# Performance work log

Hardware: AMD Instinct MI355X
Metric: run time of the kernel (lower is better)

The kernel has to match this reference:

```python
import jax, jax.numpy as jnp
import numpy as np

DIM, HEADS, SEQ_LEN = 768, 12, 4096
HEAD_DIM = DIM // HEADS
RMS_EPS = 1.1920928955078125e-07  # torch fp32 finfo eps (default for F.rms_norm)
ATTN_SCALE = 0.12


def _rms_norm(x):
    # F.rms_norm(x, (x.size(-1),)) with no weight
    return x * jax.lax.rsqrt(jnp.mean(x * x, axis=-1, keepdims=True) + RMS_EPS)


def _rotary_tables(T, head_dim):
    # angular_freq: (1/1024)**linspace(0,1,head_dim//4) padded with zeros to head_dim//2
    freqs = (1.0 / 1024.0) ** jnp.linspace(0.0, 1.0, head_dim // 4, dtype=jnp.float32)
    freqs = jnp.concatenate([freqs, jnp.zeros(head_dim // 4, dtype=jnp.float32)])
    t = jnp.arange(T, dtype=jnp.float32)
    theta = t[:, None] * freqs[None, :]  # [T, head_dim//2]
    return jnp.cos(theta), jnp.sin(theta)


def _apply_rotary(x, cos, sin):
    # x: [B, T, H, D]; cos/sin: [T, D//2]
    x1, x2 = jnp.split(x.astype(jnp.float32), 2, axis=-1)
    c = cos[None, :, None, :]
    s = sin[None, :, None, :]
    y1 = x1 * c + x2 * s
    y2 = -x1 * s + x2 * c
    return jnp.concatenate([y1, y2], axis=-1).astype(x.dtype)


def setup_inputs() -> dict:
    key = jax.random.key(0)
    k1, k2, k3 = jax.random.split(key, 3)
    x = jax.random.normal(k1, (1, SEQ_LEN, DIM), dtype=jnp.float32)
    std = 0.5 * DIM ** (-0.5)
    bound = (3.0 ** 0.5) * std
    qkv_w = jax.random.uniform(k2, (3, DIM, DIM), dtype=jnp.float32, minval=-bound, maxval=bound)
    # c_proj is zero-initialized in the module; use small random weights for a nontrivial baseline
    c_proj_w = jax.random.normal(k3, (DIM, DIM), dtype=jnp.float32) * (DIM ** -0.5)
    return {"x": x, "qkv_w": qkv_w, "c_proj_w": c_proj_w}


def reference(x, qkv_w, c_proj_w):
    B, T, dim = x.shape
    H, D = HEADS, HEAD_DIM
    # fused QKV: F.linear(x, qkv_w.flatten(end_dim=1)) -> x @ W^T, split into q,k,v
    qkv = jnp.einsum('btd,kfd->btkf', x, qkv_w)  # [B, T, 3, dim]
    qkv = qkv.reshape(B, T, 3, H, D)
    q, k, v = qkv[:, :, 0], qkv[:, :, 1], qkv[:, :, 2]  # each [B, T, H, D]
    q, k = _rms_norm(q), _rms_norm(k)
    cos, sin = _rotary_tables(T, D)
    q, k = _apply_rotary(q, cos, sin), _apply_rotary(k, cos, sin)
    # causal attention with scale=0.12 (flex_attention with causal block mask)
    scores = jnp.einsum('bthd,bshd->bhts', q, k) * ATTN_SCALE  # [B, H, T, T]
    causal = jnp.tril(jnp.ones((T, T), dtype=bool))
    scores = jnp.where(causal[None, None], scores, jnp.finfo(scores.dtype).min)
    probs = jax.nn.softmax(scores, axis=-1)
    y = jnp.einsum('bhts,bshd->bthd', probs, v).reshape(B, T, dim)
    return y @ c_proj_w.T
```

## Files before the change

kernel.cpp:

```cpp
#include <hip/hip_runtime.h>
#include <math.h>


typedef __bf16 bf16;
typedef __bf16 bf16x4 __attribute__((ext_vector_type(4)));
typedef __bf16 bf16x8 __attribute__((ext_vector_type(8)));
typedef float  f32x4  __attribute__((ext_vector_type(4)));

#define MFMA_BF16(a, b, c) __builtin_amdgcn_mfma_f32_16x16x32_bf16((a), (b), (c), 0, 0, 0)

#define SEQ  4096
#define NH   12
#define HD   64
#define DM   768
#define NQKV 2304
#define NPART 4
#define ATTN_SCALE 0.12f
#define LOG2E 1.4426950408889634f
#define RMS_EPS 1.1920928955078125e-07f

typedef __attribute__((address_space(3))) void  lds_void;
typedef const __attribute__((address_space(1))) void g_void;

__device__ __forceinline__ void gload16(const void* g, void* l)
{
  __builtin_amdgcn_global_load_lds((g_void*)g, (lds_void*)l, 16, 0, 0);
}

__global__ __launch_bounds__(256) void convert_all(
    const float* __restrict__ s0, bf16* __restrict__ d0, int n0,
    const float* __restrict__ s1, bf16* __restrict__ d1, int n1,
    const float* __restrict__ s2, bf16* __restrict__ d2, int n2)
{
  int b = blockIdx.x;
  const int b0 = n0 >> 11, b1 = n1 >> 11;
  const float* s; bf16* d;
  if (b < b0)            { s = s0; d = d0; }
  else if (b < b0 + b1)  { s = s1; d = d1; b -= b0; }
  else                   { s = s2; d = d2; b -= b0 + b1; }
  const int i0 = (b * 256 + threadIdx.x) * 8;
  f32x4 a = *(const f32x4*)(s + i0);
  f32x4 c = *(const f32x4*)(s + i0 + 4);
  bf16x8 o;
#pragma unroll
  for (int j = 0; j < 4; j++) { o[j] = (bf16)a[j]; o[j + 4] = (bf16)c[j]; }
  *(bf16x8*)(d + i0) = o;
}

__device__ __forceinline__ void gemm128_core(
    const bf16* __restrict__ A, const bf16* __restrict__ B,
    int m0, int n0, bf16 (*As)[128][32], bf16 (*Bs)[128][32], f32x4 acc[4][4])
{
  const int tid = threadIdx.x;
  const int lane = tid & 63, w = tid >> 6;
  const int c16 = lane & 15, q4 = lane >> 4;
  const int mo = (w & 1) * 64, no = (w >> 1) * 64;
  const int srow = tid >> 2, scol = (tid & 3) * 8;
  const f32x4 vzero = {0.f, 0.f, 0.f, 0.f};
#pragma unroll
  for (int i = 0; i < 4; i++)
#pragma unroll
    for (int j = 0; j < 4; j++) acc[i][j] = vzero;

  const bf16* aBase = A + (size_t)(m0 + srow) * DM + scol;
  const bf16* bBase = B + (size_t)(n0 + srow) * DM + scol;

#define STAGE128(buf, kk) do {                                          \
    gload16(aBase + (kk),                   &As[buf][srow][scol]);      \
    gload16(aBase + (size_t)64 * DM + (kk), &As[buf][srow + 64][scol]); \
    gload16(bBase + (kk),                   &Bs[buf][srow][scol]);      \
    gload16(bBase + (size_t)64 * DM + (kk), &Bs[buf][srow + 64][scol]); \
  } while (0)

  STAGE128(0, 0);
  __syncthreads();
  int cur = 0;
  for (int k0 = 0; k0 < DM; k0 += 32) {
    const int kn = k0 + 32;
    if (kn < DM) STAGE128(cur ^ 1, kn);
    bf16x8 ar[4], br[4];
#pragma unroll
    for (int mq = 0; mq < 4; mq++)
      ar[mq] = *(const bf16x8*)&As[cur][mo + mq * 16 + c16][q4 * 8];
#pragma unroll
    for (int nq = 0; nq < 4; nq++)
      br[nq] = *(const bf16x8*)&Bs[cur][no + nq * 16 + c16][q4 * 8];
    __builtin_amdgcn_s_setprio(1);
#pragma unroll
    for (int mq = 0; mq < 4; mq++)
#pragma unroll
      for (int nq = 0; nq < 4; nq++)
        acc[mq][nq] = MFMA_BF16(ar[mq], br[nq], acc[mq][nq]);
    __builtin_amdgcn_s_setprio(0);
    __syncthreads();
    cur ^= 1;
  }
#undef STAGE128
}

__global__ __launch_bounds__(256) void gemm_qkv(
    const bf16* __restrict__ A, const bf16* __restrict__ B,
    bf16* __restrict__ Qb, bf16* __restrict__ Kb, bf16* __restrict__ Vt)
{
  __shared__ bf16 As[2][128][32];
  __shared__ bf16 Bs[2][128][32];
  const int m0 = blockIdx.x * 128, n0 = blockIdx.y * 128;
  f32x4 acc[4][4];
  gemm128_core(A, B, m0, n0, As, Bs, acc);

  const int lane = threadIdx.x & 63, w = threadIdx.x >> 6;
  const int c16 = lane & 15, q4 = lane >> 4;
  const int mo = (w & 1) * 64, no = (w >> 1) * 64;
  const int kidx = blockIdx.y / 6;
  const int rr0 = (n0 - kidx * DM) + no;
  const int h = rr0 >> 6;

  if (kidx == 2) {
#pragma unroll
    for (int nq = 0; nq < 4; nq++) {
      const int d = nq * 16 + c16;
#pragma unroll
      for (int mq = 0; mq < 4; mq++) {
        const int mb = m0 + mo + mq * 16 + q4 * 4;
#pragma unroll
        for (int rg = 0; rg < 4; rg++)
          Vt[((h * HD) + d) * SEQ + mb + rg] = (bf16)acc[mq][nq][rg];
      }
    }
  } else {
    bf16* dst = kidx ? Kb : Qb;
    const float scale = kidx ? 1.0f : (ATTN_SCALE * LOG2E);
    const float fr = exp2f(-10.0f * (float)c16 * (1.0f / 15.0f));
#pragma unroll
    for (int mq = 0; mq < 4; mq++) {
#pragma unroll
      for (int rg = 0; rg < 4; rg++) {
        const int m = m0 + mo + mq * 16 + q4 * 4 + rg;
        const float x0 = acc[mq][0][rg], x1 = acc[mq][1][rg];
        const float x2 = acc[mq][2][rg], x3 = acc[mq][3][rg];
        float ss = x0 * x0 + x1 * x1 + x2 * x2 + x3 * x3;
        ss += __shfl_xor(ss, 1, 64);
        ss += __shfl_xor(ss, 2, 64);
        ss += __shfl_xor(ss, 4, 64);
        ss += __shfl_xor(ss, 8, 64);
        const float rinv = rsqrtf(ss * (1.0f / 64.0f) + RMS_EPS) * scale;
        const float xn0 = x0 * rinv, xn1 = x1 * rinv;
        const float xn2 = x2 * rinv, xn3 = x3 * rinv;
        float sn, cs;
        sincosf((float)m * fr, &sn, &cs);
        const float y0 = xn0 * cs + xn2 * sn;
        const float y2 = xn2 * cs - xn0 * sn;
        bf16* rp = dst + (size_t)(h * SEQ + m) * HD + c16;
        rp[0]  = (bf16)y0;
        rp[16] = (bf16)xn1;
        rp[32] = (bf16)y2;
        rp[48] = (bf16)xn3;
      }
    }
  }
}

__global__ __launch_bounds__(256) void gemm_proj(
    const bf16* __restrict__ A, const bf16* __restrict__ B, float* __restrict__ C)
{
  __shared__ bf16 As[2][64][32];
  __shared__ bf16 Bs[2][64][32];
  const int m0 = blockIdx.x * 64, n0 = blockIdx.y * 64;
  const int tid = threadIdx.x;
  const int lane = tid & 63, w = tid >> 6;
  const int c16 = lane & 15, q4 = lane >> 4;
  const int mo = (w & 1) * 32, no = (w >> 1) * 32;
  const int srow = tid >> 2, scol = (tid & 3) * 8;
  const f32x4 vzero = {0.f, 0.f, 0.f, 0.f};
  f32x4 acc[2][2];
#pragma unroll
  for (int i = 0; i < 2; i++)
#pragma unroll
    for (int j = 0; j < 2; j++) acc[i][j] = vzero;

  const bf16* aBase = A + (size_t)(m0 + srow) * DM + scol;
  const bf16* bBase = B + (size_t)(n0 + srow) * DM + scol;

#define STAGE64(buf, kk) do {                          \
    gload16(aBase + (kk), &As[buf][srow][scol]);       \
    gload16(bBase + (kk), &Bs[buf][srow][scol]);       \
  } while (0)

  STAGE64(0, 0);
  __syncthreads();
  int cur = 0;
  for (int k0 = 0; k0 < DM; k0 += 32) {
    const int kn = k0 + 32;
    if (kn < DM) STAGE64(cur ^ 1, kn);
    bf16x8 ar[2], br[2];
#pragma unroll
    for (int mq = 0; mq < 2; mq++)
      ar[mq] = *(const bf16x8*)&As[cur][mo + mq * 16 + c16][q4 * 8];
#pragma unroll
    for (int nq = 0; nq < 2; nq++)
      br[nq] = *(const bf16x8*)&Bs[cur][no + nq * 16 + c16][q4 * 8];
    __builtin_amdgcn_s_setprio(1);
#pragma unroll
    for (int mq = 0; mq < 2; mq++)
#pragma unroll
      for (int nq = 0; nq < 2; nq++)
        acc[mq][nq] = MFMA_BF16(ar[mq], br[nq], acc[mq][nq]);
    __builtin_amdgcn_s_setprio(0);
    __syncthreads();
    cur ^= 1;
  }
#undef STAGE64

#pragma unroll
  for (int nq = 0; nq < 2; nq++) {
    const int n = n0 + no + nq * 16 + c16;
#pragma unroll
    for (int mq = 0; mq < 2; mq++) {
      const int mb = m0 + mo + mq * 16 + q4 * 4;
#pragma unroll
      for (int rg = 0; rg < 4; rg++)
        C[(size_t)(mb + rg) * DM + n] = acc[mq][nq][rg];
    }
  }
}

__global__ __launch_bounds__(256, 3) void flash_partial(
    const bf16* __restrict__ Qb, const bf16* __restrict__ Kb,
    const bf16* __restrict__ Vt, bf16* __restrict__ Opart,
    float* __restrict__ Lpart)
{
  __shared__ bf16 Ks[64][72];
  __shared__ bf16 Vts[64][72];
  __shared__ bf16 Pst[4][32][68];
  const int id = blockIdx.x;
  const int swz = (id & 7) * 96 + (id >> 3);
  const int h = swz >> 6;
  const int rrem = swz & 63;
  const int p = rrem >> 4;
  const int jb = rrem & 15;
  const int tid = threadIdx.x;
  const int lane = tid & 63, w = tid >> 6;
  const int c16 = lane & 15, q4 = lane >> 4;
  const int sr = tid >> 3, sc8 = (tid & 7) * 8;

  const bf16* Kbase = Kb + (size_t)h * SEQ * HD;
  const bf16* Vbase = Vt + (size_t)h * HD * SEQ;
  const f32x4 vzero = {0.f, 0.f, 0.f, 0.f};

#pragma unroll 1
  for (int half = 0; half < 2; ++half) {
    const int qi = half ? jb : (31 - jb);
    const int q0 = qi * 128;

    bf16x8 aq[2][2];
#pragma unroll
    for (int f = 0; f < 2; f++) {
      const int tq = q0 + w * 32 + f * 16 + c16;
      aq[f][0] = *(const bf16x8*)&Qb[((h * SEQ) + tq) * HD + q4 * 8];
      aq[f][1] = *(const bf16x8*)&Qb[((h * SEQ) + tq) * HD + 32 + q4 * 8];
    }
    const int qg[2] = { q0 + w * 32 + c16, q0 + w * 32 + 16 + c16 };
    const int qb[2] = { q0 + w * 32,       q0 + w * 32 + 16 };

    f32x4 O[2][4];
    float l_f[2] = {0.f, 0.f};
#pragma unroll
    for (int f = 0; f < 2; f++)
#pragma unroll
      for (int j = 0; j < 4; j++) O[f][j] = vzero;

    const int sEnd = q0 + 64;
    const int sBeg = p * 64;
    if (sBeg <= sEnd) {
      bf16x8 kr0 = *(const bf16x8*)&Kbase[(sBeg + sr) * HD + sc8];
      bf16x8 kr1 = *(const bf16x8*)&Kbase[(sBeg + sr + 32) * HD + sc8];
      bf16x8 vr0 = *(const bf16x8*)&Vbase[sr * SEQ + sBeg + sc8];
      bf16x8 vr1 = *(const bf16x8*)&Vbase[(sr + 32) * SEQ + sBeg + sc8];

      for (int s0 = sBeg; s0 <= sEnd; s0 += NPART * 64) {
        __syncthreads();
        *(bf16x8*)&Ks[sr][sc8]       = kr0;
        *(bf16x8*)&Ks[sr + 32][sc8]  = kr1;
        *(bf16x8*)&Vts[sr][sc8]      = vr0;
        *(bf16x8*)&Vts[sr + 32][sc8] = vr1;
        __syncthreads();

        const int snext = s0 + NPART * 64;
        if (snext <= sEnd) {
          kr0 = *(const bf16x8*)&Kbase[(snext + sr) * HD + sc8];
          kr1 = *(const bf16x8*)&Kbase[(snext + sr + 32) * HD + sc8];
          vr0 = *(const bf16x8*)&Vbase[sr * SEQ + snext + sc8];
          vr1 = *(const bf16x8*)&Vbase[(sr + 32) * SEQ + snext + sc8];
        }

        bf16x8 kf0[4], kf1[4];
#pragma unroll
        for (int nt = 0; nt < 4; nt++) {
          kf0[nt] = *(const bf16x8*)&Ks[nt * 16 + c16][q4 * 8];
          kf1[nt] = *(const bf16x8*)&Ks[nt * 16 + c16][32 + q4 * 8];
        }
#pragma unroll
        for (int f = 0; f < 2; f++) {
          f32x4 S[4];
          __builtin_amdgcn_s_setprio(1);
#pragma unroll
          for (int nt = 0; nt < 4; nt++) {
            f32x4 z = vzero;
            z = MFMA_BF16(kf0[nt], aq[f][0], z);
            z = MFMA_BF16(kf1[nt], aq[f][1], z);
            S[nt] = z;
          }
          __builtin_amdgcn_s_setprio(0);
          float lf = l_f[f];
          if (s0 + 63 <= qb[f]) {
#pragma unroll
            for (int nt = 0; nt < 4; nt++) {
#pragma unroll
              for (int rg = 0; rg < 4; rg++) {
                const float pv = exp2f(S[nt][rg]);
                S[nt][rg] = pv;
                lf += pv;
              }
              bf16x4 pk = { (bf16)S[nt][0], (bf16)S[nt][1], (bf16)S[nt][2], (bf16)S[nt][3] };
              *(bf16x4*)&Pst[w][f * 16 + c16][nt * 16 + q4 * 4] = pk;
            }
          } else if (s0 > qb[f] + 15) {
            const bf16x4 zk = { (bf16)0.f, (bf16)0.f, (bf16)0.f, (bf16)0.f };
#pragma unroll
            for (int nt = 0; nt < 4; nt++)
              *(bf16x4*)&Pst[w][f * 16 + c16][nt * 16 + q4 * 4] = zk;
          } else {
#pragma unroll
            for (int nt = 0; nt < 4; nt++) {
#pragma unroll
              for (int rg = 0; rg < 4; rg++) {
                const int s_g = s0 + nt * 16 + q4 * 4 + rg;
                const float pv = (s_g > qg[f]) ? 0.f : exp2f(S[nt][rg]);
                S[nt][rg] = pv;
                lf += pv;
              }
              bf16x4 pk = { (bf16)S[nt][0], (bf16)S[nt][1], (bf16)S[nt][2], (bf16)S[nt][3] };
              *(bf16x4*)&Pst[w][f * 16 + c16][nt * 16 + q4 * 4] = pk;
            }
          }
          l_f[f] = lf;
        }
        bf16x8 ap[2][2];
#pragma unroll
        for (int f = 0; f < 2; f++) {
          ap[f][0] = *(const bf16x8*)&Pst[w][f * 16 + c16][q4 * 8];
          ap[f][1] = *(const bf16x8*)&Pst[w][f * 16 + c16][32 + q4 * 8];
        }
#pragma unroll
        for (int dt = 0; dt < 4; dt++) {
          bf16x8 bv0 = *(const bf16x8*)&Vts[dt * 16 + c16][q4 * 8];
          bf16x8 bv1 = *(const bf16x8*)&Vts[dt * 16 + c16][32 + q4 * 8];
          __builtin_amdgcn_s_setprio(1);
#pragma unroll
          for (int f = 0; f < 2; f++) {
            O[f][dt] = MFMA_BF16(ap[f][0], bv0, O[f][dt]);
            O[f][dt] = MFMA_BF16(ap[f][1], bv1, O[f][dt]);
          }
          __builtin_amdgcn_s_setprio(0);
        }
      }
    }

#pragma unroll
    for (int f = 0; f < 2; f++) {
      float l = l_f[f];
      l += __shfl_xor(l, 16, 64);
      l += __shfl_xor(l, 32, 64);
      l_f[f] = l;
    }
    const int u = ((h * 32 + qi) * NPART + p);
    bf16* Op = Opart + (size_t)u * 8192;
#pragma unroll
    for (int f = 0; f < 2; f++)
#pragma unroll
      for (int dt = 0; dt < 4; dt++)
#pragma unroll
        for (int rg = 0; rg < 4; rg++)
          Op[(w * 32 + f * 16 + q4 * 4 + rg) * 64 + dt * 16 + c16] = (bf16)O[f][dt][rg];
    if (lane < 32) {
      if (q4 == 0) {
#pragma unroll
        for (int f = 0; f < 2; f++)
          Lpart[u * 128 + w * 32 + f * 16 + c16] = l_f[f];
      }
    }
  }
}

__global__ __launch_bounds__(256) void flash_combine(
    const bf16* __restrict__ Opart, const float* __restrict__ Lpart,
    bf16* __restrict__ Y)
{
  const int q64 = blockIdx.x, h = blockIdx.y;
  const int qi = q64 >> 1, roff = (q64 & 1) * 64;
  const int row = threadIdx.x >> 2, cg = (threadIdx.x & 3) * 16;
  const int u0 = (h * 32 + qi) * NPART;
  const int r128 = roff + row;
  float lsum = 0.f;
#pragma unroll
  for (int p = 0; p < NPART; p++) lsum += Lpart[(u0 + p) * 128 + r128];
  const float inv = 1.0f / lsum;
  const bf16* O0 = Opart + (size_t)u0 * 8192 + r128 * 64 + cg;
  bf16* yp = Y + (size_t)(q64 * 64 + row) * DM + h * HD + cg;
#pragma unroll
  for (int j = 0; j < 16; j += 8) {
    float s[8] = {0, 0, 0, 0, 0, 0, 0, 0};
#pragma unroll
    for (int p = 0; p < NPART; p++) {
      bf16x8 a = *(const bf16x8*)(O0 + p * 8192 + j);
#pragma unroll
      for (int e = 0; e < 8; e++) s[e] += (float)a[e];
    }
#pragma unroll
    for (int e = 0; e < 8; e++) yp[j + e] = (bf16)(s[e] * inv);
  }
}

extern "C" void kernel_launch(void* const* d_in, const int* in_sizes, int n_in,
                              void* d_out, int out_size, void* d_ws, size_t ws_size,
                              hipStream_t stream)
{
  (void)in_sizes; (void)n_in; (void)out_size; (void)ws_size;
  const float* x      = (const float*)d_in[0];
  const float* qkvw   = (const float*)d_in[1];
  const float* cprojw = (const float*)d_in[2];
  float* outp = (float*)d_out;

  const int NX = SEQ * DM, NW = NQKV * DM, NP = DM * DM;

  char* ws = (char*)d_ws;
  bf16*  xb    = (bf16*)(ws);
  bf16*  wqkv  = (bf16*)(ws + 6291456);
  bf16*  wproj = (bf16*)(ws + 9830400);
  bf16*  Q     = (bf16*)(ws + 11010048);
  bf16*  K     = (bf16*)(ws + 17301504);
  bf16*  Vt    = (bf16*)(ws + 23592960);
  bf16*  Y     = (bf16*)(ws + 29884416);
  bf16*  Opart = (bf16*)(ws + 36175872);
  float* Lpart = (float*)(ws + 61341696);

  convert_all<<<dim3((NX + NW + NP) / 2048), 256, 0, stream>>>(
      x, xb, NX, qkvw, wqkv, NW, cprojw, wproj, NP);

  gemm_qkv     <<<dim3(SEQ / 128, NQKV / 128), 256, 0, stream>>>(xb, wqkv, Q, K, Vt);
  flash_partial<<<dim3(16 * NH * NPART),       256, 0, stream>>>(Q, K, Vt, Opart, Lpart);
  flash_combine<<<dim3(SEQ / 64, NH),          256, 0, stream>>>(Opart, Lpart, Y);
  gemm_proj    <<<dim3(SEQ / 64, DM / 64),     256, 0, stream>>>(Y, wproj, outp);
}
```

Before: 161.9 us.

## Split KV into five partitions and compute softmax row sums via MFMA

Raises the number of KV partitions per query tile from four to five, adjusting the block swizzle and the workspace offset of the partial row-sum buffer. It also drops the scalar per-element row-sum accumulation and cross-lane shuffles, and instead gets the row sums from extra MFMAs that multiply the probability tile by a ones-column vector. The extra partition adds parallelism and shortens each block's serial KV loop, at the cost of more partial outputs to write and combine. The MFMA row sum takes the additions off the VALU but uses bf16-rounded probabilities and adds four matrix ops per tile.

```diff
diff --git a/kernel.cpp b/kernel.cpp
--- a/kernel.cpp
+++ b/kernel.cpp
@@ -14,7 +14,7 @@
 #define HD   64
 #define DM   768
 #define NQKV 2304
-#define NPART 4
+#define NPART 5
 #define ATTN_SCALE 0.12f
 #define LOG2E 1.4426950408889634f
 #define RMS_EPS 1.1920928955078125e-07f
@@ -233,9 +233,9 @@
   __shared__ bf16 Vts[64][72];
   __shared__ bf16 Pst[4][32][68];
   const int id = blockIdx.x;
-  const int swz = (id & 7) * 96 + (id >> 3);
-  const int h = swz >> 6;
-  const int rrem = swz & 63;
+  const int swz = (id & 7) * 120 + (id >> 3);
+  const int h = swz / 80;
+  const int rrem = swz - h * 80;
   const int p = rrem >> 4;
   const int jb = rrem & 15;
   const int tid = threadIdx.x;
@@ -247,6 +247,11 @@
   const bf16* Vbase = Vt + (size_t)h * HD * SEQ;
   const f32x4 vzero = {0.f, 0.f, 0.f, 0.f};
 
+  const bf16 bv1c = (c16 == 0) ? (bf16)1.0f : (bf16)0.0f;
+  bf16x8 bone;
+#pragma unroll
+  for (int e = 0; e < 8; e++) bone[e] = bv1c;
+
 #pragma unroll 1
   for (int half = 0; half < 2; ++half) {
     const int qi = half ? jb : (31 - jb);
@@ -263,7 +268,7 @@
     const int qb[2] = { q0 + w * 32,       q0 + w * 32 + 16 };
 
     f32x4 O[2][4];
-    float l_f[2] = {0.f, 0.f};
+    f32x4 acc_l[2] = {vzero, vzero};
 #pragma unroll
     for (int f = 0; f < 2; f++)
 #pragma unroll
@@ -311,16 +316,11 @@
             S[nt] = z;
           }
           __builtin_amdgcn_s_setprio(0);
-          float lf = l_f[f];
           if (s0 + 63 <= qb[f]) {
 #pragma unroll
             for (int nt = 0; nt < 4; nt++) {
 #pragma unroll
-              for (int rg = 0; rg < 4; rg++) {
-                const float pv = exp2f(S[nt][rg]);
-                S[nt][rg] = pv;
-                lf += pv;
-              }
+              for (int rg = 0; rg < 4; rg++) S[nt][rg] = exp2f(S[nt][rg]);
               bf16x4 pk = { (bf16)S[nt][0], (bf16)S[nt][1], (bf16)S[nt][2], (bf16)S[nt][3] };
               *(bf16x4*)&Pst[w][f * 16 + c16][nt * 16 + q4 * 4] = pk;
             }
@@ -335,15 +335,12 @@
 #pragma unroll
               for (int rg = 0; rg < 4; rg++) {
                 const int s_g = s0 + nt * 16 + q4 * 4 + rg;
-                const float pv = (s_g > qg[f]) ? 0.f : exp2f(S[nt][rg]);
-                S[nt][rg] = pv;
-                lf += pv;
+                S[nt][rg] = (s_g > qg[f]) ? 0.f : exp2f(S[nt][rg]);
               }
               bf16x4 pk = { (bf16)S[nt][0], (bf16)S[nt][1], (bf16)S[nt][2], (bf16)S[nt][3] };
               *(bf16x4*)&Pst[w][f * 16 + c16][nt * 16 + q4 * 4] = pk;
             }
           }
-          l_f[f] = lf;
         }
         bf16x8 ap[2][2];
 #pragma unroll
@@ -352,27 +349,25 @@
           ap[f][1] = *(const bf16x8*)&Pst[w][f * 16 + c16][32 + q4 * 8];
         }
 #pragma unroll
+        for (int f = 0; f < 2; f++) {
+          acc_l[f] = MFMA_BF16(ap[f][0], bone, acc_l[f]);
+          acc_l[f] = MFMA_BF16(ap[f][1], bone, acc_l[f]);
+        }
+#pragma unroll
         for (int dt = 0; dt < 4; dt++) {
           bf16x8 bv0 = *(const bf16x8*)&Vts[dt * 16 + c16][q4 * 8];
-          bf16x8 bv1 = *(const bf16x8*)&Vts[dt * 16 + c16][32 + q4 * 8];
+          bf16x8 bw1 = *(const bf16x8*)&Vts[dt * 16 + c16][32 + q4 * 8];
           __builtin_amdgcn_s_setprio(1);
 #pragma unroll
           for (int f = 0; f < 2; f++) {
             O[f][dt] = MFMA_BF16(ap[f][0], bv0, O[f][dt]);
-            O[f][dt] = MFMA_BF16(ap[f][1], bv1, O[f][dt]);
+            O[f][dt] = MFMA_BF16(ap[f][1], bw1, O[f][dt]);
           }
           __builtin_amdgcn_s_setprio(0);
         }
       }
     }
 
-#pragma unroll
-    for (int f = 0; f < 2; f++) {
-      float l = l_f[f];
-      l += __shfl_xor(l, 16, 64);
-      l += __shfl_xor(l, 32, 64);
-      l_f[f] = l;
-    }
     const int u = ((h * 32 + qi) * NPART + p);
     bf16* Op = Opart + (size_t)u * 8192;
 #pragma unroll
@@ -382,12 +377,12 @@
 #pragma unroll
         for (int rg = 0; rg < 4; rg++)
           Op[(w * 32 + f * 16 + q4 * 4 + rg) * 64 + dt * 16 + c16] = (bf16)O[f][dt][rg];
-    if (lane < 32) {
-      if (q4 == 0) {
-#pragma unroll
-        for (int f = 0; f < 2; f++)
-          Lpart[u * 128 + w * 32 + f * 16 + c16] = l_f[f];
-      }
+    if (c16 == 0) {
+#pragma unroll
+      for (int f = 0; f < 2; f++)
+#pragma unroll
+        for (int rg = 0; rg < 4; rg++)
+          Lpart[u * 128 + w * 32 + f * 16 + q4 * 4 + rg] = acc_l[f][rg];
     }
   }
 }
@@ -442,7 +437,7 @@
   bf16*  Vt    = (bf16*)(ws + 23592960);
   bf16*  Y     = (bf16*)(ws + 29884416);
   bf16*  Opart = (bf16*)(ws + 36175872);
-  float* Lpart = (float*)(ws + 61341696);
+  float* Lpart = (float*)(ws + 67633152);
 
   convert_all<<<dim3((NX + NW + NP) / 2048), 256, 0, stream>>>(
       x, xb, NX, qkvw, wqkv, NW, cprojw, wproj, NP);
```

Result: no change. 164.8 us (+1.8%).
